# Optimization experiments

Hardware: AMD Instinct MI355X
Metric: run time of the kernel (lower is better)

The kernel has to match this reference:

```python
import jax, jax.numpy as jnp
import numpy as np

B, T, DM = 2, 512, 1024
H, DH = 16, 64          # n_heads, d_head = d_model // n_heads
D, R = 32, 4            # d_manifold, metric_net rank
TEMP_MIN = 0.5


def _rope_tables(t_len, d_head):
    inv_freq = 1.0 / (10000.0 ** (jnp.arange(0, d_head, 2, dtype=jnp.float32) / d_head))
    t = jnp.arange(t_len, dtype=jnp.float32)
    freqs = t[:, None] * inv_freq[None, :]          # [T, d_head//2]
    emb = jnp.concatenate([freqs, freqs], axis=-1)  # [T, d_head]
    return jnp.cos(emb), jnp.sin(emb)


def _apply_rope(x, cos, sin):
    # x: [B, H, T, d_head]
    half = x.shape[-1] // 2
    x1, x2 = x[..., :half], x[..., half:]
    c1 = cos[None, None, :, :half]
    s1 = sin[None, None, :, :half]
    return jnp.concatenate([x1 * c1 - x2 * s1, x1 * s1 + x2 * c1], axis=-1)


def setup_inputs() -> dict:
    key = jax.random.key(0)
    ks = jax.random.split(key, 9)
    s = 0.02
    return {
        "x": jax.random.normal(ks[0], (B, T, DM), dtype=jnp.float32),
        "Wq": s * jax.random.normal(ks[1], (DM, DM), dtype=jnp.float32),
        "Wk": s * jax.random.normal(ks[2], (DM, DM), dtype=jnp.float32),
        "Wv": s * jax.random.normal(ks[3], (DM, DM), dtype=jnp.float32),
        "Wo": s * jax.random.normal(ks[4], (DM, DM), dtype=jnp.float32),
        "Wqm": s * jax.random.normal(ks[5], (DH, D), dtype=jnp.float32),
        "Wkm": s * jax.random.normal(ks[6], (DH, D), dtype=jnp.float32),
        "Wmetric": s * jax.random.normal(ks[7], (D, D * R), dtype=jnp.float32),
        "temperature": jnp.asarray(1.0, dtype=jnp.float32),
    }


def reference(x, Wq, Wk, Wv, Wo, Wqm, Wkm, Wmetric, temperature):
    b, t, c = x.shape
    # projections -> [B, H, T, d_head]
    def split_heads(y):
        return y.reshape(b, t, H, DH).transpose(0, 2, 1, 3)
    q = split_heads(x @ Wq)
    k = split_heads(x @ Wk)
    v = split_heads(x @ Wv)

    cos, sin = _rope_tables(t, DH)
    q = _apply_rope(q, cos, sin)
    k = _apply_rope(k, cos, sin)

    # manifold coordinates in (0,1): [B, H, T, D]
    qm = jax.nn.sigmoid(jnp.einsum('bhtd,dm->bhtm', q, Wqm))
    km = jax.nn.sigmoid(jnp.einsum('bhtd,dm->bhtm', k, Wkm))

    # low-rank metric factor U(q): [B, H, T, D, R]
    U = jnp.einsum('bhtm,mn->bhtn', qm, Wmetric).reshape(b, H, t, D, R)

    # Euclidean part: ||q_i - k_j||^2 = |q|^2 + |k|^2 - 2 q.k  -> [B,H,T,T]
    q2 = jnp.sum(qm * qm, axis=-1)
    k2 = jnp.sum(km * km, axis=-1)
    qk = jnp.einsum('bhid,bhjd->bhij', qm, km)
    dist_euc = q2[..., :, None] + k2[..., None, :] - 2.0 * qk

    # low-rank part: ||U_i^T (q_i - k_j)||^2, factorized as U_i^T q_i - U_i^T k_j
    Uq = jnp.einsum('bhidr,bhid->bhir', U, qm)          # [B,H,T,R]
    Uk = jnp.einsum('bhidr,bhjd->bhijr', U, km)         # [B,H,T,T,R]
    dist_lr = jnp.sum((Uq[:, :, :, None, :] - Uk) ** 2, axis=-1)

    dist_sq = jnp.maximum(dist_euc + dist_lr, 0.0)

    temp = jnp.maximum(temperature, TEMP_MIN)
    attn = -dist_sq / temp

    causal = jnp.triu(jnp.ones((t, t), dtype=bool), k=1)
    attn = jnp.where(causal[None, None], -jnp.inf, attn)
    attn = jax.nn.softmax(attn, axis=-1)

    out = jnp.einsum('bhij,bhjd->bhid', attn, v)        # [B,H,T,d_head]
    out = out.transpose(0, 2, 1, 3).reshape(b, t, c)
    return out @ Wo
```

## Files before the change

### kernel.cpp

```cpp
#include <hip/hip_runtime.h>
#include <cmath>

constexpr int B_  = 2;
constexpr int T_  = 512;
constexpr int DM_ = 1024;
constexpr int H_  = 16;
constexpr int DH_ = 64;
constexpr int D_  = 32;
constexpr int R_  = 4;
constexpr int BH_ = B_ * H_;

typedef __bf16 bf16x8 __attribute__((ext_vector_type(8)));
typedef float  f32x4  __attribute__((ext_vector_type(4)));
typedef unsigned short u16x8 __attribute__((ext_vector_type(8)));

__device__ __forceinline__ unsigned short f2bf(float f) {
    unsigned u = __float_as_uint(f);
    return (unsigned short)((u + 0x7fffu + ((u >> 16) & 1u)) >> 16);
}
__device__ __forceinline__ float bf2f(unsigned short v) {
    return __uint_as_float((unsigned)v << 16);
}

__device__ __forceinline__ void gload16(const void* g, void* l) {
    __builtin_amdgcn_global_load_lds(
        (const __attribute__((address_space(1))) void*)g,
        (__attribute__((address_space(3))) void*)l, 16, 0, 0);
}

__global__ __launch_bounds__(256) void prep_kernel(
    const float* __restrict__ x,
    const float* __restrict__ Wq, const float* __restrict__ Wk,
    const float* __restrict__ Wv, const float* __restrict__ Wo,
    unsigned short* __restrict__ xb,
    unsigned short* __restrict__ wqb, unsigned short* __restrict__ wkb,
    unsigned short* __restrict__ wvb, unsigned short* __restrict__ wob)
{
    const int t = threadIdx.x;
    const int z = blockIdx.z;
    if (z == 4) {
        int base = (blockIdx.y * 16 + blockIdx.x) * 4096 + t * 16;
#pragma unroll
        for (int c = 0; c < 4; ++c) {
            float4 v = *(const float4*)&x[base + c * 4];
            ushort4 o = { f2bf(v.x), f2bf(v.y), f2bf(v.z), f2bf(v.w) };
            *(ushort4*)&xb[base + c * 4] = o;
        }
        return;
    }
    __shared__ __align__(16) unsigned short Ls[64][72];
    const float* W = (z == 0) ? Wq : (z == 1) ? Wk : (z == 2) ? Wv : Wo;
    unsigned short* O = (z == 0) ? wqb : (z == 1) ? wkb : (z == 2) ? wvb : wob;
    const int k0 = blockIdx.x * 64;
    const int n0 = blockIdx.y * 64;
#pragma unroll
    for (int it = 0; it < 4; ++it) {
        int r = it * 16 + (t >> 4);
        int c = (t & 15) * 4;
        float4 v4 = *(const float4*)&W[(size_t)(k0 + r) * DM_ + n0 + c];
        Ls[c + 0][r] = f2bf(v4.x); Ls[c + 1][r] = f2bf(v4.y);
        Ls[c + 2][r] = f2bf(v4.z); Ls[c + 3][r] = f2bf(v4.w);
    }
    __syncthreads();
#pragma unroll
    for (int it = 0; it < 2; ++it) {
        int nl = it * 32 + (t >> 3);
        int kc = (t & 7) * 8;
        *(u16x8*)&O[(size_t)(n0 + nl) * DM_ + k0 + kc] = *(const u16x8*)&Ls[nl][kc];
    }
}

__global__ __launch_bounds__(256) void qkv_feat_gemm(
    const unsigned short* __restrict__ A,
    const unsigned short* __restrict__ wqb, const unsigned short* __restrict__ wkb,
    const unsigned short* __restrict__ wvb,
    const float* __restrict__ Wqm, const float* __restrict__ Wkm,
    const float* __restrict__ Wmetric,
    unsigned short* __restrict__ a_hi, unsigned short* __restrict__ a_lo,
    unsigned short* __restrict__ km_hi, unsigned short* __restrict__ km_lo,
    float* __restrict__ q2p, float* __restrict__ k2,
    unsigned short* __restrict__ Urb, unsigned short* __restrict__ vT)
{
    __shared__ union {
        struct { __align__(16) unsigned short As[64 * 32];
                 __align__(16) unsigned short Bs[64 * 32]; } g;
        struct { float Ct[64][65]; float qm[64][33]; } f;
    } sh;

    const int tid  = threadIdx.x;
    const int lane = tid & 63;
    const int w    = tid >> 6;
    const int wm   = (w & 1) * 32;
    const int wn   = (w >> 1) * 32;
    const int l15  = lane & 15, quad = lane >> 4;

    const int bm = blockIdx.y * 64;
    const int n0 = blockIdx.x * 64;
    const int which = n0 >> 10;
    const int bn = n0 & 1023;
    const int h  = bn >> 6;
    const unsigned short* Bt = (which == 0) ? wqb : (which == 1) ? wkb : wvb;

    f32x4 acc[2][2] = {};
    const int sr = tid >> 2;
    const int sc = (tid & 3) * 8;
    const unsigned short* Ap = A  + (size_t)(bm + sr) * DM_ + sc;
    const unsigned short* Bp = Bt + (size_t)(bn + sr) * DM_ + sc;
    unsigned short* AsP = &sh.g.As[sr * 32 + sc];
    unsigned short* BsP = &sh.g.Bs[sr * 32 + sc];

    for (int k0 = 0; k0 < DM_; k0 += 32) {
        gload16(Ap + k0, AsP);
        gload16(Bp + k0, BsP);
        __syncthreads();
        bf16x8 af[2], bfr[2];
#pragma unroll
        for (int i = 0; i < 2; ++i) {
            af[i]  = *(const bf16x8*)&sh.g.As[(wm + i * 16 + l15) * 32 + quad * 8];
            bfr[i] = *(const bf16x8*)&sh.g.Bs[(wn + i * 16 + l15) * 32 + quad * 8];
        }
#pragma unroll
        for (int mi = 0; mi < 2; ++mi)
#pragma unroll
            for (int ni = 0; ni < 2; ++ni)
                acc[mi][ni] = __builtin_amdgcn_mfma_f32_16x16x32_bf16(
                    af[mi], bfr[ni], acc[mi][ni], 0, 0, 0);
        __syncthreads();
    }

    if (which == 2) {
#pragma unroll
        for (int mi = 0; mi < 2; ++mi)
#pragma unroll
            for (int ni = 0; ni < 2; ++ni) {
                f32x4 a = acc[mi][ni];
                int d = wn + ni * 16 + l15;
#pragma unroll
                for (int r = 0; r < 4; ++r) {
                    int m = bm + wm + mi * 16 + quad * 4 + r;
                    int bb = m >> 9, tt = m & (T_ - 1);
                    vT[(((size_t)bb * H_ + h) * DH_ + d) * T_ + tt] = f2bf(a[r]);
                }
            }
        return;
    }

#pragma unroll
    for (int mi = 0; mi < 2; ++mi)
#pragma unroll
        for (int ni = 0; ni < 2; ++ni) {
            f32x4 a = acc[mi][ni];
            int cl = wn + ni * 16 + l15;
#pragma unroll
            for (int r = 0; r < 4; ++r)
                sh.f.Ct[wm + mi * 16 + quad * 4 + r][cl] = a[r];
        }
    __syncthreads();

    for (int e = tid; e < 2048; e += 256) {
        int row = e >> 5, d = e & 31;
        int t = (bm + row) & (T_ - 1);
        float ang = (float)t * expf((float)d * -0.28782313662425575f);
        float s, c;
        sincosf(ang, &s, &c);
        float v1 = sh.f.Ct[row][d], v2 = sh.f.Ct[row][d + 32];
        sh.f.Ct[row][d]      = v1 * c - v2 * s;
        sh.f.Ct[row][d + 32] = v1 * s + v2 * c;
    }
    __syncthreads();

    const float* Wm = (which == 0) ? Wqm : Wkm;
    const int r  = tid >> 2, c = tid & 3, mg = c * 8;
    float a8[8] = {};
    for (int d = 0; d < 64; ++d) {
        float qr = sh.f.Ct[r][d];
        float4 w0 = *(const float4*)&Wm[d * 32 + mg];
        float4 w1 = *(const float4*)&Wm[d * 32 + mg + 4];
        a8[0] = fmaf(qr, w0.x, a8[0]); a8[1] = fmaf(qr, w0.y, a8[1]);
        a8[2] = fmaf(qr, w0.z, a8[2]); a8[3] = fmaf(qr, w0.w, a8[3]);
        a8[4] = fmaf(qr, w1.x, a8[4]); a8[5] = fmaf(qr, w1.y, a8[5]);
        a8[6] = fmaf(qr, w1.z, a8[6]); a8[7] = fmaf(qr, w1.w, a8[7]);
    }
#pragma unroll
    for (int j = 0; j < 8; ++j) a8[j] = 1.0f / (1.0f + __expf(-a8[j]));

    const int m_ = bm + r;
    const int b_ = m_ >> 9, t_ = m_ & (T_ - 1);
    const int bh = b_ * H_ + h;
    const size_t rowg = (size_t)bh * T_ + t_;

    if (which == 1) {
        u16x8 hi8, lo8;
#pragma unroll
        for (int j = 0; j < 8; ++j) {
            unsigned short hv = f2bf(a8[j]);
            hi8[j] = hv; lo8[j] = f2bf(a8[j] - bf2f(hv));
        }
        *(u16x8*)&km_hi[rowg * 32 + mg] = hi8;
        *(u16x8*)&km_lo[rowg * 32 + mg] = lo8;
        float p = 0.f;
#pragma unroll
        for (int j = 0; j < 8; ++j) p = fmaf(a8[j], a8[j], p);
        p += __shfl_xor(p, 1); p += __shfl_xor(p, 2);
        if (c == 0) k2[rowg] = p;
        return;
    }

#pragma unroll
    for (int j = 0; j < 8; ++j) sh.f.qm[r][mg + j] = a8[j];
    __syncthreads();

    const int nc = c * 32;
    float U[32] = {};
    for (int m = 0; m < 32; ++m) {
        float qv = sh.f.qm[r][m];
        const float* wrow = &Wmetric[m * 128 + nc];
#pragma unroll
        for (int n4 = 0; n4 < 8; ++n4) {
            float4 wv = *(const float4*)&wrow[n4 * 4];
            U[n4 * 4 + 0] = fmaf(qv, wv.x, U[n4 * 4 + 0]);
            U[n4 * 4 + 1] = fmaf(qv, wv.y, U[n4 * 4 + 1]);
            U[n4 * 4 + 2] = fmaf(qv, wv.z, U[n4 * 4 + 2]);
            U[n4 * 4 + 3] = fmaf(qv, wv.w, U[n4 * 4 + 3]);
        }
    }
    float uq[4] = {};
#pragma unroll
    for (int n = 0; n < 32; ++n) {
        int nn = nc + n, d = nn >> 2, rr = nn & 3;
        Urb[((size_t)(bh * R_ + rr) * T_ + t_) * D_ + d] = f2bf(U[n]);
        uq[rr] = fmaf(U[n], sh.f.qm[r][d], uq[rr]);
    }
#pragma unroll
    for (int rr = 0; rr < 4; ++rr) {
        uq[rr] += __shfl_xor(uq[rr], 1);
        uq[rr] += __shfl_xor(uq[rr], 2);
    }
    u16x8 hi8, lo8;
    float p = 0.f;
#pragma unroll
    for (int j = 0; j < 8; ++j) {
        float qmv = sh.f.qm[r][mg + j];
        float av = qmv + uq[0] * U[j * 4 + 0] + uq[1] * U[j * 4 + 1]
                       + uq[2] * U[j * 4 + 2] + uq[3] * U[j * 4 + 3];
        unsigned short hv = f2bf(av);
        hi8[j] = hv; lo8[j] = f2bf(av - bf2f(hv));
        p = fmaf(qmv, qmv, p);
    }
    *(u16x8*)&a_hi[rowg * 32 + mg] = hi8;
    *(u16x8*)&a_lo[rowg * 32 + mg] = lo8;
    p += __shfl_xor(p, 1); p += __shfl_xor(p, 2);
    if (c == 0)
        q2p[rowg] = p + uq[0] * uq[0] + uq[1] * uq[1]
                      + uq[2] * uq[2] + uq[3] * uq[3];
}

__global__ __launch_bounds__(256) void out_gemm64(
    const unsigned short* __restrict__ A, const unsigned short* __restrict__ Bt,
    float* __restrict__ C)
{
    __shared__ __align__(16) unsigned short As[64 * 32];
    __shared__ __align__(16) unsigned short Bs[64 * 32];
    const int tid  = threadIdx.x;
    const int lane = tid & 63;
    const int w    = tid >> 6;
    const int wm   = (w & 1) * 32;
    const int wn   = (w >> 1) * 32;
    const int bm = blockIdx.y * 64;
    const int bn = blockIdx.x * 64;

    f32x4 acc[2][2] = {};
    const int sr = tid >> 2;
    const int sc = (tid & 3) * 8;
    const unsigned short* Ap = A  + (size_t)(bm + sr) * DM_ + sc;
    const unsigned short* Bp = Bt + (size_t)(bn + sr) * DM_ + sc;
    unsigned short* AsP = &As[sr * 32 + sc];
    unsigned short* BsP = &Bs[sr * 32 + sc];
    const int fr = lane & 15;
    const int fq = (lane >> 4) * 8;

    for (int k0 = 0; k0 < DM_; k0 += 32) {
        gload16(Ap + k0, AsP);
        gload16(Bp + k0, BsP);
        __syncthreads();
        bf16x8 af[2], bfr[2];
#pragma unroll
        for (int i = 0; i < 2; ++i) {
            af[i]  = *(const bf16x8*)&As[(wm + i * 16 + fr) * 32 + fq];
            bfr[i] = *(const bf16x8*)&Bs[(wn + i * 16 + fr) * 32 + fq];
        }
#pragma unroll
        for (int mi = 0; mi < 2; ++mi)
#pragma unroll
            for (int ni = 0; ni < 2; ++ni)
                acc[mi][ni] = __builtin_amdgcn_mfma_f32_16x16x32_bf16(
                    af[mi], bfr[ni], acc[mi][ni], 0, 0, 0);
        __syncthreads();
    }
#pragma unroll
    for (int mi = 0; mi < 2; ++mi)
#pragma unroll
        for (int ni = 0; ni < 2; ++ni) {
            f32x4 a = acc[mi][ni];
            int col = bn + wn + ni * 16 + (lane & 15);
#pragma unroll
            for (int r = 0; r < 4; ++r) {
                int row = bm + wm + mi * 16 + (lane >> 4) * 4 + r;
                C[(size_t)row * DM_ + col] = a[r];
            }
        }
}

constexpr int PROW = 40;
__global__ __launch_bounds__(256) void attn_mfma(
    const unsigned short* __restrict__ a_hi, const unsigned short* __restrict__ a_lo,
    const unsigned short* __restrict__ km_hi, const unsigned short* __restrict__ km_lo,
    const unsigned short* __restrict__ Urb,
    const float* __restrict__ q2p, const float* __restrict__ k2,
    const float* __restrict__ temp_p, const unsigned short* __restrict__ vT,
    unsigned short* __restrict__ ctxb)
{
    __shared__ __align__(16) unsigned short P_lds[4][32 * PROW];
    __shared__ __align__(16) float OP[4][32][64];
    __shared__ float ML[4][32];

    const int itile = blockIdx.x, bh = blockIdx.y;
    const int i0 = itile * 32;
    const int tid = threadIdx.x, w = tid >> 6, lane = tid & 63;
    const int l15 = lane & 15, quad = lane >> 4;

    const float inv_temp = 1.0f / fmaxf(temp_p[0], 0.5f);

    bf16x8 Ahi[2], Alo[2], Aur[4][2];
#pragma unroll
    for (int mi = 0; mi < 2; ++mi) {
        size_t ab = ((size_t)bh * T_ + i0 + mi * 16 + l15) * 32 + quad * 8;
        Ahi[mi] = *(const bf16x8*)&a_hi[ab];
        Alo[mi] = *(const bf16x8*)&a_lo[ab];
#pragma unroll
        for (int r = 0; r < 4; ++r)
            Aur[r][mi] = *(const bf16x8*)
                &Urb[(((size_t)bh * R_ + r) * T_ + i0 + mi * 16 + l15) * 32 + quad * 8];
    }
    float q2r[2][4];
#pragma unroll
    for (int mi = 0; mi < 2; ++mi)
#pragma unroll
        for (int rg = 0; rg < 4; ++rg)
            q2r[mi][rg] = q2p[(size_t)bh * T_ + i0 + mi * 16 + quad * 4 + rg];

    f32x4 Oacc[2][4] = {};
    float psum[2][4] = {};

    for (int jt = w; jt <= itile; jt += 4) {
        const int j0 = jt * 32;
        bf16x8 Bhi[2], Blo[2];
#pragma unroll
        for (int ni = 0; ni < 2; ++ni) {
            size_t kb = ((size_t)bh * T_ + j0 + ni * 16 + l15) * 32 + quad * 8;
            Bhi[ni] = *(const bf16x8*)&km_hi[kb];
            Blo[ni] = *(const bf16x8*)&km_lo[kb];
        }
        f32x4 acc[2][2] = {};
#pragma unroll
        for (int mi = 0; mi < 2; ++mi)
#pragma unroll
            for (int ni = 0; ni < 2; ++ni) {
                acc[mi][ni] = __builtin_amdgcn_mfma_f32_16x16x32_bf16(
                    Alo[mi], Bhi[ni], acc[mi][ni], 0, 0, 0);
                acc[mi][ni] = __builtin_amdgcn_mfma_f32_16x16x32_bf16(
                    Ahi[mi], Blo[ni], acc[mi][ni], 0, 0, 0);
                acc[mi][ni] = __builtin_amdgcn_mfma_f32_16x16x32_bf16(
                    Ahi[mi], Bhi[ni], acc[mi][ni], 0, 0, 0);
            }
        f32x4 sq[2][2] = {};
#pragma unroll
        for (int r = 0; r < 4; ++r) {
            f32x4 ar[2][2] = {};
#pragma unroll
            for (int mi = 0; mi < 2; ++mi)
#pragma unroll
                for (int ni = 0; ni < 2; ++ni)
                    ar[mi][ni] = __builtin_amdgcn_mfma_f32_16x16x32_bf16(
                        Aur[r][mi], Bhi[ni], ar[mi][ni], 0, 0, 0);
#pragma unroll
            for (int mi = 0; mi < 2; ++mi)
#pragma unroll
                for (int ni = 0; ni < 2; ++ni)
                    sq[mi][ni] += ar[mi][ni] * ar[mi][ni];
        }
        float k2c[2];
#pragma unroll
        for (int ni = 0; ni < 2; ++ni)
            k2c[ni] = k2[(size_t)bh * T_ + j0 + ni * 16 + l15];
        const bool diag = (jt == itile);
#pragma unroll
        for (int mi = 0; mi < 2; ++mi)
#pragma unroll
            for (int ni = 0; ni < 2; ++ni)
#pragma unroll
                for (int rg = 0; rg < 4; ++rg) {
                    float dist = q2r[mi][rg] + k2c[ni]
                               - 2.f * acc[mi][ni][rg] + sq[mi][ni][rg];
                    float sc = -fmaxf(dist, 0.f) * inv_temp;
                    if (diag && (ni * 16 + l15) > (mi * 16 + quad * 4 + rg))
                        sc = -1e30f;
                    float p = __expf(sc);
                    psum[mi][rg] += p;
                    P_lds[w][(mi * 16 + quad * 4 + rg) * PROW + ni * 16 + l15] = f2bf(p);
                }
        bf16x8 Pf[2], Vf[4];
#pragma unroll
        for (int mi = 0; mi < 2; ++mi)
            Pf[mi] = *(const bf16x8*)&P_lds[w][(mi * 16 + l15) * PROW + quad * 8];
#pragma unroll
        for (int n4 = 0; n4 < 4; ++n4)
            Vf[n4] = *(const bf16x8*)
                &vT[((size_t)bh * DH_ + n4 * 16 + l15) * T_ + j0 + quad * 8];
#pragma unroll
        for (int mi = 0; mi < 2; ++mi)
#pragma unroll
            for (int n4 = 0; n4 < 4; ++n4)
                Oacc[mi][n4] = __builtin_amdgcn_mfma_f32_16x16x32_bf16(
                    Pf[mi], Vf[n4], Oacc[mi][n4], 0, 0, 0);
    }

#pragma unroll
    for (int mi = 0; mi < 2; ++mi)
#pragma unroll
        for (int rg = 0; rg < 4; ++rg) {
            float v = psum[mi][rg];
            v += __shfl_xor(v, 1); v += __shfl_xor(v, 2);
            v += __shfl_xor(v, 4); v += __shfl_xor(v, 8);
            psum[mi][rg] = v;
        }
    if (l15 == 0)
#pragma unroll
        for (int mi = 0; mi < 2; ++mi)
#pragma unroll
            for (int rg = 0; rg < 4; ++rg)
                ML[w][mi * 16 + quad * 4 + rg] = psum[mi][rg];
#pragma unroll
    for (int mi = 0; mi < 2; ++mi)
#pragma unroll
        for (int n4 = 0; n4 < 4; ++n4)
#pragma unroll
            for (int rg = 0; rg < 4; ++rg)
                OP[w][mi * 16 + quad * 4 + rg][n4 * 16 + l15] = Oacc[mi][n4][rg];
    __syncthreads();

    const int ii = tid >> 3, ds = tid & 7;
    float l = ML[0][ii] + ML[1][ii] + ML[2][ii] + ML[3][ii];
    float O[8] = {};
#pragma unroll
    for (int wv = 0; wv < 4; ++wv) {
        float4 o0 = *(const float4*)&OP[wv][ii][ds * 8];
        float4 o1 = *(const float4*)&OP[wv][ii][ds * 8 + 4];
        O[0] += o0.x; O[1] += o0.y; O[2] += o0.z; O[3] += o0.w;
        O[4] += o1.x; O[5] += o1.y; O[6] += o1.z; O[7] += o1.w;
    }
    const float inv = 1.0f / l;
    const int b = bh >> 4, h = bh & 15;
    u16x8 o;
#pragma unroll
    for (int dd = 0; dd < 8; ++dd) o[dd] = f2bf(O[dd] * inv);
    *(u16x8*)&ctxb[((size_t)b * T_ + i0 + ii) * DM_ + h * 64 + ds * 8] = o;
}

extern "C" void kernel_launch(void* const* d_in, const int* in_sizes, int n_in,
                              void* d_out, int out_size, void* d_ws, size_t ws_size,
                              hipStream_t stream)
{
    const float* x       = (const float*)d_in[0];
    const float* Wq      = (const float*)d_in[1];
    const float* Wk      = (const float*)d_in[2];
    const float* Wv      = (const float*)d_in[3];
    const float* Wo      = (const float*)d_in[4];
    const float* Wqm     = (const float*)d_in[5];
    const float* Wkm     = (const float*)d_in[6];
    const float* Wmetric = (const float*)d_in[7];
    const float* temp    = (const float*)d_in[8];
    float* out = (float*)d_out;
    float* ws  = (float*)d_ws;

    float* q2p = ws;
    float* k2  = q2p + (size_t)BH_ * T_;
    unsigned short* xb   = (unsigned short*)(k2 + (size_t)BH_ * T_);
    unsigned short* wqb  = xb   + (size_t)DM_ * DM_;
    unsigned short* wkb  = wqb  + (size_t)DM_ * DM_;
    unsigned short* wvb  = wkb  + (size_t)DM_ * DM_;
    unsigned short* wob  = wvb  + (size_t)DM_ * DM_;
    unsigned short* a_hi = wob  + (size_t)DM_ * DM_;
    unsigned short* a_lo = a_hi + (size_t)BH_ * T_ * D_;
    unsigned short* kmhi = a_lo + (size_t)BH_ * T_ * D_;
    unsigned short* kmlo = kmhi + (size_t)BH_ * T_ * D_;
    unsigned short* Urb  = kmlo + (size_t)BH_ * T_ * D_;
    unsigned short* vT   = Urb  + (size_t)BH_ * R_ * T_ * D_;
    unsigned short* ctxb = vT   + (size_t)BH_ * DH_ * T_;

    prep_kernel<<<dim3(16, 16, 5), 256, 0, stream>>>(
        x, Wq, Wk, Wv, Wo, xb, wqb, wkb, wvb, wob);
    qkv_feat_gemm<<<dim3(48, 16), 256, 0, stream>>>(
        xb, wqb, wkb, wvb, Wqm, Wkm, Wmetric,
        a_hi, a_lo, kmhi, kmlo, q2p, k2, Urb, vT);
    attn_mfma<<<dim3(T_ / 32, BH_), 256, 0, stream>>>(
        a_hi, a_lo, kmhi, kmlo, Urb, q2p, k2, temp, vT, ctxb);
    out_gemm64<<<dim3(16, 16), 256, 0, stream>>>(ctxb, wob, out);
}
```

Measured before the change: 175.4 us.

## Double GEMM K-tile with XOR-swizzled LDS and restructure feature epilogue per-wave

Both the QKV and output GEMMs now stage 64-wide K tiles with an XOR swizzle, halving the number of barrier-separated iterations and reducing LDS bank conflicts. The feature epilogue that computes manifold coordinates, the metric factor and its projections is rewritten so each wave handles one row at a time with lanes mapped to output features, replacing per-thread register arrays of 32 U values. This aims to cut loop and sync overhead and register pressure, at the cost of more LDS use, more serialised per-row work and scalar (non-vector) global stores in the epilogue.

After: 159.2 us. -9.2%, faster.

```diff
diff --git a/kernel.cpp b/kernel.cpp
--- a/kernel.cpp
+++ b/kernel.cpp
@@ -21,7 +21,6 @@
 __device__ __forceinline__ float bf2f(unsigned short v) {
     return __uint_as_float((unsigned)v << 16);
 }
-
 __device__ __forceinline__ void gload16(const void* g, void* l) {
     __builtin_amdgcn_global_load_lds(
         (const __attribute__((address_space(1))) void*)g,
@@ -82,9 +81,10 @@
     unsigned short* __restrict__ Urb, unsigned short* __restrict__ vT)
 {
     __shared__ union {
-        struct { __align__(16) unsigned short As[64 * 32];
-                 __align__(16) unsigned short Bs[64 * 32]; } g;
-        struct { float Ct[64][65]; float qm[64][33]; } f;
+        struct { __align__(16) unsigned short As[64 * 64];
+                 __align__(16) unsigned short Bs[64 * 64]; } g;
+        struct { float Ct[64][65];
+                 float qms[4][32]; float Us[4][128]; float Uqs[4][4]; } f;
     } sh;
 
     const int tid  = threadIdx.x;
@@ -101,30 +101,43 @@
     const int h  = bn >> 6;
     const unsigned short* Bt = (which == 0) ? wqb : (which == 1) ? wkb : wvb;
 
+    const int srow = tid >> 3, kcs = tid & 7, kcg = kcs ^ (srow & 7);
+    const unsigned short* Ap0 = A  + (size_t)(bm + srow) * DM_ + kcg * 8;
+    const unsigned short* Bp0 = Bt + (size_t)(bn + srow) * DM_ + kcg * 8;
+    const unsigned short* Ap1 = Ap0 + 32 * DM_;
+    const unsigned short* Bp1 = Bp0 + 32 * DM_;
+    unsigned short* As0 = &sh.g.As[tid * 8];
+    unsigned short* Bs0 = &sh.g.Bs[tid * 8];
+    unsigned short* As1 = As0 + 2048;
+    unsigned short* Bs1 = Bs0 + 2048;
+
     f32x4 acc[2][2] = {};
-    const int sr = tid >> 2;
-    const int sc = (tid & 3) * 8;
-    const unsigned short* Ap = A  + (size_t)(bm + sr) * DM_ + sc;
-    const unsigned short* Bp = Bt + (size_t)(bn + sr) * DM_ + sc;
-    unsigned short* AsP = &sh.g.As[sr * 32 + sc];
-    unsigned short* BsP = &sh.g.Bs[sr * 32 + sc];
-
-    for (int k0 = 0; k0 < DM_; k0 += 32) {
-        gload16(Ap + k0, AsP);
-        gload16(Bp + k0, BsP);
+    for (int k0 = 0; k0 < DM_; k0 += 64) {
+        gload16(Ap0 + k0, As0);
+        gload16(Ap1 + k0, As1);
+        gload16(Bp0 + k0, Bs0);
+        gload16(Bp1 + k0, Bs1);
         __syncthreads();
-        bf16x8 af[2], bfr[2];
-#pragma unroll
-        for (int i = 0; i < 2; ++i) {
-            af[i]  = *(const bf16x8*)&sh.g.As[(wm + i * 16 + l15) * 32 + quad * 8];
-            bfr[i] = *(const bf16x8*)&sh.g.Bs[(wn + i * 16 + l15) * 32 + quad * 8];
-        }
-#pragma unroll
-        for (int mi = 0; mi < 2; ++mi)
-#pragma unroll
-            for (int ni = 0; ni < 2; ++ni)
-                acc[mi][ni] = __builtin_amdgcn_mfma_f32_16x16x32_bf16(
-                    af[mi], bfr[ni], acc[mi][ni], 0, 0, 0);
+        bf16x8 af[2][2], bfr[2][2];
+#pragma unroll
+        for (int ki = 0; ki < 2; ++ki)
+#pragma unroll
+            for (int i = 0; i < 2; ++i) {
+                int ra = wm + i * 16 + l15;
+                int rb = wn + i * 16 + l15;
+                int kch = ki * 4 + quad;
+                af[ki][i]  = *(const bf16x8*)&sh.g.As[ra * 64 + (kch ^ (ra & 7)) * 8];
+                bfr[ki][i] = *(const bf16x8*)&sh.g.Bs[rb * 64 + (kch ^ (rb & 7)) * 8];
+            }
+#pragma unroll
+        for (int mi = 0; mi < 2; ++mi)
+#pragma unroll
+            for (int ni = 0; ni < 2; ++ni) {
+                acc[mi][ni] = __builtin_amdgcn_mfma_f32_16x16x32_bf16(
+                    af[0][mi], bfr[0][ni], acc[mi][ni], 0, 0, 0);
+                acc[mi][ni] = __builtin_amdgcn_mfma_f32_16x16x32_bf16(
+                    af[1][mi], bfr[1][ni], acc[mi][ni], 0, 0, 0);
+            }
         __syncthreads();
     }
 
@@ -137,8 +150,8 @@
                 int d = wn + ni * 16 + l15;
 #pragma unroll
                 for (int r = 0; r < 4; ++r) {
-                    int m = bm + wm + mi * 16 + quad * 4 + r;
-                    int bb = m >> 9, tt = m & (T_ - 1);
+                    int row = bm + wm + mi * 16 + quad * 4 + r;
+                    int bb = row >> 9, tt = row & (T_ - 1);
                     vT[(((size_t)bb * H_ + h) * DH_ + d) * T_ + tt] = f2bf(a[r]);
                 }
             }
@@ -170,145 +183,77 @@
     __syncthreads();
 
     const float* Wm = (which == 0) ? Wqm : Wkm;
-    const int r  = tid >> 2, c = tid & 3, mg = c * 8;
-    float a8[8] = {};
-    for (int d = 0; d < 64; ++d) {
-        float qr = sh.f.Ct[r][d];
-        float4 w0 = *(const float4*)&Wm[d * 32 + mg];
-        float4 w1 = *(const float4*)&Wm[d * 32 + mg + 4];
-        a8[0] = fmaf(qr, w0.x, a8[0]); a8[1] = fmaf(qr, w0.y, a8[1]);
-        a8[2] = fmaf(qr, w0.z, a8[2]); a8[3] = fmaf(qr, w0.w, a8[3]);
-        a8[4] = fmaf(qr, w1.x, a8[4]); a8[5] = fmaf(qr, w1.y, a8[5]);
-        a8[6] = fmaf(qr, w1.z, a8[6]); a8[7] = fmaf(qr, w1.w, a8[7]);
-    }
-#pragma unroll
-    for (int j = 0; j < 8; ++j) a8[j] = 1.0f / (1.0f + __expf(-a8[j]));
-
-    const int m_ = bm + r;
-    const int b_ = m_ >> 9, t_ = m_ & (T_ - 1);
-    const int bh = b_ * H_ + h;
-    const size_t rowg = (size_t)bh * T_ + t_;
-
-    if (which == 1) {
-        u16x8 hi8, lo8;
-#pragma unroll
-        for (int j = 0; j < 8; ++j) {
-            unsigned short hv = f2bf(a8[j]);
-            hi8[j] = hv; lo8[j] = f2bf(a8[j] - bf2f(hv));
-        }
-        *(u16x8*)&km_hi[rowg * 32 + mg] = hi8;
-        *(u16x8*)&km_lo[rowg * 32 + mg] = lo8;
-        float p = 0.f;
-#pragma unroll
-        for (int j = 0; j < 8; ++j) p = fmaf(a8[j], a8[j], p);
-        p += __shfl_xor(p, 1); p += __shfl_xor(p, 2);
-        if (c == 0) k2[rowg] = p;
-        return;
-    }
-
-#pragma unroll
-    for (int j = 0; j < 8; ++j) sh.f.qm[r][mg + j] = a8[j];
-    __syncthreads();
-
-    const int nc = c * 32;
-    float U[32] = {};
-    for (int m = 0; m < 32; ++m) {
-        float qv = sh.f.qm[r][m];
-        const float* wrow = &Wmetric[m * 128 + nc];
-#pragma unroll
-        for (int n4 = 0; n4 < 8; ++n4) {
-            float4 wv = *(const float4*)&wrow[n4 * 4];
-            U[n4 * 4 + 0] = fmaf(qv, wv.x, U[n4 * 4 + 0]);
-            U[n4 * 4 + 1] = fmaf(qv, wv.y, U[n4 * 4 + 1]);
-            U[n4 * 4 + 2] = fmaf(qv, wv.z, U[n4 * 4 + 2]);
-            U[n4 * 4 + 3] = fmaf(qv, wv.w, U[n4 * 4 + 3]);
-        }
-    }
-    float uq[4] = {};
-#pragma unroll
-    for (int n = 0; n < 32; ++n) {
-        int nn = nc + n, d = nn >> 2, rr = nn & 3;
-        Urb[((size_t)(bh * R_ + rr) * T_ + t_) * D_ + d] = f2bf(U[n]);
-        uq[rr] = fmaf(U[n], sh.f.qm[r][d], uq[rr]);
-    }
-#pragma unroll
-    for (int rr = 0; rr < 4; ++rr) {
-        uq[rr] += __shfl_xor(uq[rr], 1);
-        uq[rr] += __shfl_xor(uq[rr], 2);
-    }
-    u16x8 hi8, lo8;
-    float p = 0.f;
-#pragma unroll
-    for (int j = 0; j < 8; ++j) {
-        float qmv = sh.f.qm[r][mg + j];
-        float av = qmv + uq[0] * U[j * 4 + 0] + uq[1] * U[j * 4 + 1]
-                       + uq[2] * U[j * 4 + 2] + uq[3] * U[j * 4 + 3];
-        unsigned short hv = f2bf(av);
-        hi8[j] = hv; lo8[j] = f2bf(av - bf2f(hv));
-        p = fmaf(qmv, qmv, p);
-    }
-    *(u16x8*)&a_hi[rowg * 32 + mg] = hi8;
-    *(u16x8*)&a_lo[rowg * 32 + mg] = lo8;
-    p += __shfl_xor(p, 1); p += __shfl_xor(p, 2);
-    if (c == 0)
-        q2p[rowg] = p + uq[0] * uq[0] + uq[1] * uq[1]
-                      + uq[2] * uq[2] + uq[3] * uq[3];
-}
-
-__global__ __launch_bounds__(256) void out_gemm64(
-    const unsigned short* __restrict__ A, const unsigned short* __restrict__ Bt,
-    float* __restrict__ C)
-{
-    __shared__ __align__(16) unsigned short As[64 * 32];
-    __shared__ __align__(16) unsigned short Bs[64 * 32];
-    const int tid  = threadIdx.x;
-    const int lane = tid & 63;
-    const int w    = tid >> 6;
-    const int wm   = (w & 1) * 32;
-    const int wn   = (w >> 1) * 32;
-    const int bm = blockIdx.y * 64;
-    const int bn = blockIdx.x * 64;
-
-    f32x4 acc[2][2] = {};
-    const int sr = tid >> 2;
-    const int sc = (tid & 3) * 8;
-    const unsigned short* Ap = A  + (size_t)(bm + sr) * DM_ + sc;
-    const unsigned short* Bp = Bt + (size_t)(bn + sr) * DM_ + sc;
-    unsigned short* AsP = &As[sr * 32 + sc];
-    unsigned short* BsP = &Bs[sr * 32 + sc];
-    const int fr = lane & 15;
-    const int fq = (lane >> 4) * 8;
-
-    for (int k0 = 0; k0 < DM_; k0 += 32) {
-        gload16(Ap + k0, AsP);
-        gload16(Bp + k0, BsP);
-        __syncthreads();
-        bf16x8 af[2], bfr[2];
-#pragma unroll
-        for (int i = 0; i < 2; ++i) {
-            af[i]  = *(const bf16x8*)&As[(wm + i * 16 + fr) * 32 + fq];
-            bfr[i] = *(const bf16x8*)&Bs[(wn + i * 16 + fr) * 32 + fq];
-        }
-#pragma unroll
-        for (int mi = 0; mi < 2; ++mi)
-#pragma unroll
-            for (int ni = 0; ni < 2; ++ni)
-                acc[mi][ni] = __builtin_amdgcn_mfma_f32_16x16x32_bf16(
-                    af[mi], bfr[ni], acc[mi][ni], 0, 0, 0);
-        __syncthreads();
-    }
-#pragma unroll
-    for (int mi = 0; mi < 2; ++mi)
-#pragma unroll
-        for (int ni = 0; ni < 2; ++ni) {
-            f32x4 a = acc[mi][ni];
-            int col = bn + wn + ni * 16 + (lane & 15);
-#pragma unroll
-            for (int r = 0; r < 4; ++r) {
-                int row = bm + wm + mi * 16 + (lane >> 4) * 4 + r;
-                C[(size_t)row * DM_ + col] = a[r];
-            }
-        }
+    for (int rr = w; rr < 64; rr += 4) {
+        const int m_ = bm + rr;
+        const int b_ = m_ >> 9, t_ = m_ & (T_ - 1);
+        const int bh = b_ * H_ + h;
+        const size_t rowg = (size_t)bh * T_ + t_;
+
+        float qmv = 0.f;
+        if (lane < 32) {
+            float acc2 = 0.f;
+#pragma unroll 8
+            for (int d = 0; d < 64; ++d)
+                acc2 += sh.f.Ct[rr][d] * Wm[d * 32 + lane];
+            qmv = 1.0f / (1.0f + __expf(-acc2));
+            sh.f.qms[w][lane] = qmv;
+        }
+
+        if (which == 1) {
+            if (lane < 32) {
+                unsigned short hv = f2bf(qmv);
+                km_hi[rowg * 32 + lane] = hv;
+                km_lo[rowg * 32 + lane] = f2bf(qmv - bf2f(hv));
+                float p = qmv * qmv;
+                p += __shfl_xor(p, 1);  p += __shfl_xor(p, 2);
+                p += __shfl_xor(p, 4);  p += __shfl_xor(p, 8);
+                p += __shfl_xor(p, 16);
+                if (lane == 0) k2[rowg] = p;
+            }
+            continue;
+        }
+
+        float a0 = 0.f, a1 = 0.f;
+#pragma unroll 8
+        for (int m = 0; m < 32; ++m) {
+            float qv = sh.f.qms[w][m];
+            a0 += qv * Wmetric[m * 128 + lane];
+            a1 += qv * Wmetric[m * 128 + 64 + lane];
+        }
+        sh.f.Us[w][lane] = a0; sh.f.Us[w][64 + lane] = a1;
+        {
+            int r0 = lane & 3, d0 = lane >> 2, d1 = 16 + (lane >> 2);
+            Urb[(((size_t)bh * R_ + r0) * T_ + t_) * D_ + d0] = f2bf(a0);
+            Urb[(((size_t)bh * R_ + r0) * T_ + t_) * D_ + d1] = f2bf(a1);
+        }
+        if (lane < 4) {
+            float acc2 = 0.f;
+#pragma unroll
+            for (int d = 0; d < 32; ++d)
+                acc2 += sh.f.Us[w][d * 4 + lane] * sh.f.qms[w][d];
+            sh.f.Uqs[w][lane] = acc2;
+        }
+        if (lane < 32) {
+            float b = sh.f.Uqs[w][0] * sh.f.Us[w][lane * 4 + 0]
+                    + sh.f.Uqs[w][1] * sh.f.Us[w][lane * 4 + 1]
+                    + sh.f.Uqs[w][2] * sh.f.Us[w][lane * 4 + 2]
+                    + sh.f.Uqs[w][3] * sh.f.Us[w][lane * 4 + 3];
+            float a = sh.f.qms[w][lane] + b;
+            unsigned short hv = f2bf(a);
+            a_hi[rowg * 32 + lane] = hv;
+            a_lo[rowg * 32 + lane] = f2bf(a - bf2f(hv));
+        }
+        if (lane == 0) {
+            float acc2 = 0.f;
+#pragma unroll
+            for (int m = 0; m < 32; ++m)
+                acc2 += sh.f.qms[w][m] * sh.f.qms[w][m];
+#pragma unroll
+            for (int r = 0; r < 4; ++r)
+                acc2 += sh.f.Uqs[w][r] * sh.f.Uqs[w][r];
+            q2p[rowg] = acc2;
+        }
+    }
 }
 
 constexpr int PROW = 40;
@@ -465,6 +410,74 @@
 #pragma unroll
     for (int dd = 0; dd < 8; ++dd) o[dd] = f2bf(O[dd] * inv);
     *(u16x8*)&ctxb[((size_t)b * T_ + i0 + ii) * DM_ + h * 64 + ds * 8] = o;
+}
+
+__global__ __launch_bounds__(256) void out_gemm_bk64(
+    const unsigned short* __restrict__ A, const unsigned short* __restrict__ Bt,
+    float* __restrict__ C)
+{
+    __shared__ __align__(16) unsigned short As[64 * 64];
+    __shared__ __align__(16) unsigned short Bs[64 * 64];
+    const int tid  = threadIdx.x;
+    const int lane = tid & 63;
+    const int w    = tid >> 6;
+    const int wm   = (w & 1) * 32;
+    const int wn   = (w >> 1) * 32;
+    const int l15  = lane & 15, quad = lane >> 4;
+    const int bm = blockIdx.y * 64;
+    const int bn = blockIdx.x * 64;
+
+    const int srow = tid >> 3, kcs = tid & 7, kcg = kcs ^ (srow & 7);
+    const unsigned short* Ap0 = A  + (size_t)(bm + srow) * DM_ + kcg * 8;
+    const unsigned short* Bp0 = Bt + (size_t)(bn + srow) * DM_ + kcg * 8;
+    const unsigned short* Ap1 = Ap0 + 32 * DM_;
+    const unsigned short* Bp1 = Bp0 + 32 * DM_;
+    unsigned short* As0 = &As[tid * 8];
+    unsigned short* Bs0 = &Bs[tid * 8];
+    unsigned short* As1 = As0 + 2048;
+    unsigned short* Bs1 = Bs0 + 2048;
+
+    f32x4 acc[2][2] = {};
+    for (int k0 = 0; k0 < DM_; k0 += 64) {
+        gload16(Ap0 + k0, As0);
+        gload16(Ap1 + k0, As1);
+        gload16(Bp0 + k0, Bs0);
+        gload16(Bp1 + k0, Bs1);
+        __syncthreads();
+        bf16x8 af[2][2], bfr[2][2];
+#pragma unroll
+        for (int ki = 0; ki < 2; ++ki)
+#pragma unroll
+            for (int i = 0; i < 2; ++i) {
+                int ra = wm + i * 16 + l15;
+                int rb = wn + i * 16 + l15;
+                int kch = ki * 4 + quad;
+                af[ki][i]  = *(const bf16x8*)&As[ra * 64 + (kch ^ (ra & 7)) * 8];
+                bfr[ki][i] = *(const bf16x8*)&Bs[rb * 64 + (kch ^ (rb & 7)) * 8];
+            }
+#pragma unroll
+        for (int mi = 0; mi < 2; ++mi)
+#pragma unroll
+            for (int ni = 0; ni < 2; ++ni) {
+                acc[mi][ni] = __builtin_amdgcn_mfma_f32_16x16x32_bf16(
+                    af[0][mi], bfr[0][ni], acc[mi][ni], 0, 0, 0);
+                acc[mi][ni] = __builtin_amdgcn_mfma_f32_16x16x32_bf16(
+                    af[1][mi], bfr[1][ni], acc[mi][ni], 0, 0, 0);
+            }
+        __syncthreads();
+    }
+#pragma unroll
+    for (int mi = 0; mi < 2; ++mi)
+#pragma unroll
+        for (int ni = 0; ni < 2; ++ni) {
+            f32x4 a = acc[mi][ni];
+            int col = bn + wn + ni * 16 + l15;
+#pragma unroll
+            for (int r = 0; r < 4; ++r) {
+                int row = bm + wm + mi * 16 + quad * 4 + r;
+                C[(size_t)row * DM_ + col] = a[r];
+            }
+        }
 }
 
 extern "C" void kernel_launch(void* const* d_in, const int* in_sizes, int n_in,
@@ -505,5 +518,5 @@
         a_hi, a_lo, kmhi, kmlo, q2p, k2, Urb, vT);
     attn_mfma<<<dim3(T_ / 32, BH_), 256, 0, stream>>>(
         a_hi, a_lo, kmhi, kmlo, Urb, q2p, k2, temp, vT, ctxb);
-    out_gemm64<<<dim3(16, 16), 256, 0, stream>>>(ctxb, wob, out);
-}
+    out_gemm_bk64<<<dim3(16, 16), 256, 0, stream>>>(ctxb, wob, out);
+}
```
